# Optimization experiments

Measured on AMD Instinct MI355X. Metric: run time of the kernel, lower is better.

Reference implementation:

```python
import jax, jax.numpy as jnp
import numpy as np

B, S, D_IN = 64, 3072, 128
E, H, OUT = 64, 256, 10
K, STRIDE = 3, 3
T_OUT = (S - K) // STRIDE + 1  # 1024


def setup_inputs() -> dict:
    key = jax.random.key(0)
    ks = jax.random.split(key, 8)
    inputs = jax.random.normal(ks[0], (B, S, D_IN), dtype=jnp.float32)
    r = jnp.zeros((B, E, T_OUT), dtype=jnp.float32)
    s = 0.05
    conv_w = jax.random.normal(ks[1], (E, D_IN, K), dtype=jnp.float32) * s
    conv_b = jax.random.normal(ks[2], (E,), dtype=jnp.float32) * s
    w_ih = jax.random.normal(ks[3], (4 * H, E), dtype=jnp.float32) * s
    w_hh = jax.random.normal(ks[4], (4 * H, H), dtype=jnp.float32) * s
    b_ih = jax.random.normal(ks[5], (4 * H,), dtype=jnp.float32) * s
    b_hh = jax.random.normal(ks[6], (4 * H,), dtype=jnp.float32) * s
    lin_w = jax.random.normal(ks[7], (OUT, H), dtype=jnp.float32) * s
    lin_b = jnp.zeros((OUT,), dtype=jnp.float32)
    return {"inputs": inputs, "r": r, "batch_size": B,
            "conv_w": conv_w, "conv_b": conv_b,
            "w_ih": w_ih, "w_hh": w_hh, "b_ih": b_ih, "b_hh": b_hh,
            "lin_w": lin_w, "lin_b": lin_b}


def _forward(inputs, conv_w, conv_b, w_ih, w_hh, b_ih, b_hh, lin_w, lin_b):
    # F.normalize(inputs, dim=2): L2-normalize feature dim (eps=1e-12)
    norm = jnp.linalg.norm(inputs, axis=2, keepdims=True)
    x = inputs / jnp.maximum(norm, 1e-12)
    # permute(0,2,1): [B, D_IN, S], then Conv1d stride 3
    x = jnp.transpose(x, (0, 2, 1))
    emb = jax.lax.conv_general_dilated(
        x, conv_w, window_strides=(STRIDE,), padding='VALID',
        dimension_numbers=('NCH', 'OIH', 'NCH'))
    emb = emb + conv_b[None, :, None]
    act = jax.nn.relu(emb)                      # [B, E, T_OUT]
    xs = jnp.transpose(act, (2, 0, 1))          # [T, B, E] for scan

    def step(carry, x_t):
        h, c = carry
        gates = x_t @ w_ih.T + b_ih + h @ w_hh.T + b_hh  # [B, 4H]
        i_g, f_g, g_g, o_g = jnp.split(gates, 4, axis=1)
        c_new = jax.nn.sigmoid(f_g) * c + jax.nn.sigmoid(i_g) * jnp.tanh(g_g)
        h_new = jax.nn.sigmoid(o_g) * jnp.tanh(c_new)
        return (h_new, c_new), None

    h0 = jnp.zeros((inputs.shape[0], H), dtype=inputs.dtype)
    c0 = jnp.zeros((inputs.shape[0], H), dtype=inputs.dtype)
    (h_last, _), _ = jax.lax.scan(step, (h0, c0), xs)
    return h_last @ lin_w.T + lin_b             # [B, OUT]


def reference(inputs, r, batch_size, conv_w, conv_b, w_ih, w_hh, b_ih, b_hh, lin_w, lin_b):
    # mode='plain': r and batch_size are unused by the math
    return _forward(inputs, conv_w, conv_b, w_ih, w_hh, b_ih, b_hh, lin_w, lin_b)
```

## Files before the change

### kernel.cpp

```cpp
#include <hip/hip_runtime.h>
#include <math.h>

#define B_   64
#define S_   3072
#define DIN  128
#define E_   64
#define H_   256
#define OUT_ 10
#define T_   1024
#define NG   32
#define GB   2
#define NCH  8
#define NLINES 192
#define SLOT 168

#define ACT_BYTES   (B_*E_*T_*4)
#define HBUF_OFF    ACT_BYTES
#define HBUF_BYTES  (NG*2*NLINES*16)
#define HFINAL_OFF  (HBUF_OFF + HBUF_BYTES)
#define HFINAL_BYTES (NG*GB*H_*4)

typedef float f32x4 __attribute__((ext_vector_type(4)));

__device__ __forceinline__ f32x4 coh_load_f32x4(const float* p) {
  f32x4 r;
  asm volatile("global_load_dwordx4 %0, %1, off sc0 sc1\n\ts_waitcnt vmcnt(0)"
               : "=v"(r) : "v"(p) : "memory");
  return r;
}
__device__ __forceinline__ void coh_store_f32x4(float* p, f32x4 v) {
  asm volatile("global_store_dwordx4 %0, %1, off sc0 sc1" :: "v"(p), "v"(v) : "memory");
}

__device__ __forceinline__ void step_barrier() {
  asm volatile("s_waitcnt lgkmcnt(0)" ::: "memory");
  __builtin_amdgcn_sched_barrier(0);
  __builtin_amdgcn_s_barrier();
}

__device__ __forceinline__ float fast_sigmoid(float x) {
  return __builtin_amdgcn_rcpf(1.0f + __expf(-x));
}
__device__ __forceinline__ float fast_tanh(float x) {
  return 2.0f * __builtin_amdgcn_rcpf(1.0f + __expf(-2.0f * x)) - 1.0f;
}

__global__ __launch_bounds__(512, 1) void conv_kernel(
    const float* __restrict__ in,
    const float* __restrict__ cw,
    const float* __restrict__ cb,
    float* __restrict__ actT)
{
  extern __shared__ float xs[];
  float4* xs4 = (float4*)xs;
  const int bid = blockIdx.x;
  const int b  = bid >> 4;
  const int tb = bid & 15;
  const int tid = threadIdx.x;

  const float4* gin = (const float4*)(in + (size_t)b*S_*DIN + (size_t)tb*192*DIN);
  #pragma unroll
  for (int i = 0; i < 12; ++i) {
    int f4 = tid + i*512;
    int r = f4 >> 5, dq = f4 & 31;
    xs4[r*32 + (dq ^ (r & 7))] = gin[f4];
  }
  __syncthreads();

  const int wv = tid >> 6, ln = tid & 63;
  for (int rr = 0; rr < 24; ++rr) {
    int r = wv*24 + rr;
    int u = r*32 + ((ln >> 1) ^ (r & 7));
    float2* p = (float2*)((char*)xs + (size_t)u*16 + (size_t)(ln & 1)*8);
    float2 v = *p;
    float s = v.x*v.x + v.y*v.y;
    #pragma unroll
    for (int off = 32; off >= 1; off >>= 1) s += __shfl_xor(s, off);
    float inv = 1.0f / fmaxf(sqrtf(s), 1e-12f);
    v.x *= inv; v.y *= inv;
    *p = v;
  }
  __syncthreads();

  const int eo = __builtin_amdgcn_readfirstlane(wv);
  float acc[8];
  #pragma unroll
  for (int j = 0; j < 8; ++j) acc[j] = cb[eo*8 + j];

  const int r0 = 3*ln, r1 = 3*ln + 1, r2 = 3*ln + 2;
  #pragma unroll 4
  for (int dq = 0; dq < 32; ++dq) {
    float4 x0 = xs4[r0*32 + (dq ^ (r0 & 7))];
    float4 x1 = xs4[r1*32 + (dq ^ (r1 & 7))];
    float4 x2 = xs4[r2*32 + (dq ^ (r2 & 7))];
    #pragma unroll
    for (int j = 0; j < 8; ++j) {
      const float* wp = cw + (size_t)(eo*8 + j)*(DIN*3) + dq*12;
      acc[j] += x0.x*wp[0] + x1.x*wp[1] + x2.x*wp[2]
              + x0.y*wp[3] + x1.y*wp[4] + x2.y*wp[5]
              + x0.z*wp[6] + x1.z*wp[7] + x2.z*wp[8]
              + x0.w*wp[9] + x1.w*wp[10] + x2.w*wp[11];
    }
  }

  const int tg = tb*64 + ln;
  #pragma unroll
  for (int j = 0; j < 8; ++j) {
    int e = eo*8 + j;
    actT[(size_t)b*E_*T_ + (size_t)e*T_ + tg] = fmaxf(acc[j], 0.0f);
  }
}

__device__ __forceinline__ void kmap(int hidx, int& kh, int& slot) {
  kh = (hidx < 160) ? 0 : 1;
  slot = (hidx < 160) ? hidx : hidx - 160;
}

__global__ __launch_bounds__(512, 1) void lstm_kernel(
    const float* __restrict__ actT,
    const float* __restrict__ w_ih,
    const float* __restrict__ w_hh,
    const float* __restrict__ b_ih,
    const float* __restrict__ b_hh,
    float* hbuf,
    float* hfinal)
{
  __shared__ float sl[2][2][2][SLOT];

  const int bid = blockIdx.x;
  const int g = bid & 31;
  const int q = bid >> 5;
  const int tid = threadIdx.x;
  const int w = tid >> 6;
  const int l = tid & 63;

  const int khalf = l & 1;
  const int m     = (l >> 1) & 3;
  const int o     = l >> 3;
  const int b     = w & 1;
  const int wh    = w >> 1;
  const int hh    = wh*8 + o;
  const int row   = m*256 + 32*q + hh;

  float4 wv[40];
  if (khalf == 0) {
    const float4* ph = (const float4*)(w_hh + (size_t)row*H_);
    #pragma unroll
    for (int i = 0; i < 40; ++i) wv[i] = ph[i];
  } else {
    const float4* ph = (const float4*)(w_hh + (size_t)row*H_) + 40;
    #pragma unroll
    for (int i = 0; i < 24; ++i) wv[i] = ph[i];
    const float4* px = (const float4*)(w_ih + (size_t)row*E_);
    #pragma unroll
    for (int i = 0; i < 16; ++i) wv[24+i] = px[i];
  }
  const float bias = (khalf == 0) ? (b_ih[row] + b_hh[row]) : 0.0f;

  for (int i = tid; i < 2*2*2*SLOT; i += 512) ((float*)sl)[i] = 0.0f;

  const int ss = l / 24;
  const bool is_store = ((l % 24) == 0);
  const int sline = q*24 + w*3 + ss;
  const int shh0 = wh*8 + 3*ss;
  const int scnt = (ss == 2) ? 2 : 3;

  const bool lane_ok = ((l % 24) != 0);
  const int rank = l - 1 - (l >= 24) - (l >= 48);
  const int pi = w*61 + rank;
  const bool is_poll = (w < 3) && lane_ok && (pi < 168);
  int pline = 0, pb = 0, phh0 = 0, pcnt = 3;
  if (is_poll) {
    int qq = pi / 24;
    int pq = qq + (qq >= q ? 1 : 0);
    int rest = pi % 24;
    int pw = rest / 3, ps = rest % 3;
    pline = pq*24 + pw*3 + ps;
    pb = pw & 1;
    phh0 = 32*pq + (pw >> 1)*8 + 3*ps;
    pcnt = (ps == 2) ? 2 : 3;
  }

  const bool is_x = (tid >= 384);
  const int xi = tid - 384, xb = (xi >> 6) & 1, xe = xi & 63;
  const float* actp = actT + (size_t)((g*GB + xb)*E_ + xe)*T_;

  float* hb = hbuf + (size_t)g*(2*NLINES*4);

  if (is_x) sl[0][xb][1][96 + xe] = actp[0];
  __syncthreads();

  float c = 0.0f;
  for (int t = 0; t < T_; ++t) {
    const int p = t & 1;

    float xval = 0.0f;
    if (is_x) xval = actp[t];

    if (t > 0 && is_poll) {
      const float* lp = hb + (size_t)(p*NLINES + pline)*4;
      f32x4 v = coh_load_f32x4(lp);
      while (__float_as_int(v[3]) != t) v = coh_load_f32x4(lp);
      #pragma unroll
      for (int j = 0; j < 3; ++j) {
        if (j < pcnt) {
          int kh, slot; kmap(phh0 + j, kh, slot);
          sl[p][pb][kh][slot] = v[j];
        }
      }
    }
    if (is_x) sl[p][xb][1][96 + xe] = xval;
    step_barrier();

    float acc = bias;
    {
      const float* hs = &sl[p][b][khalf][0];
      #pragma unroll
      for (int i = 0; i < 40; ++i) {
        float4 h4 = *(const float4*)(hs + i*4);
        acc += wv[i].x*h4.x + wv[i].y*h4.y + wv[i].z*h4.z + wv[i].w*h4.w;
      }
    }

    float ksum = acc + __shfl_xor(acc, 1);
    float x1 = __shfl_xor(ksum, 2);
    float x2 = __shfl_xor(ksum, 4);
    float x3 = __shfl_xor(x1, 4);
    float gi = (m==0)?ksum:(m==1)?x1 :(m==2)?x2 :x3;
    float gf = (m==0)?x1 :(m==1)?ksum:(m==2)?x3 :x2;
    float gg = (m==0)?x2 :(m==1)?x3 :(m==2)?ksum:x1;
    float go = (m==0)?x3 :(m==1)?x2 :(m==2)?x1 :ksum;

    float si = fast_sigmoid(gi);
    float sf = fast_sigmoid(gf);
    float so = fast_sigmoid(go);
    c = sf*c + si*fast_tanh(gg);
    float h = so*fast_tanh(c);

    float v1 = __shfl(h, (l + 8) & 63, 64);
    float v2 = __shfl(h, (l + 16) & 63, 64);
    if (is_store) {
      f32x4 line;
      line[0] = h; line[1] = v1; line[2] = v2;
      line[3] = __int_as_float(t + 1);
      float* dp = hb + (size_t)((((t+1) & 1)*NLINES) + sline)*4;
      coh_store_f32x4(dp, line);
      #pragma unroll
      for (int j = 0; j < 3; ++j) {
        if (j < scnt) {
          int kh, slot; kmap(32*q + shh0 + j, kh, slot);
          sl[p ^ 1][b][kh][slot] = (j == 0) ? h : (j == 1) ? v1 : v2;
        }
      }
      if (t == T_ - 1) {
        #pragma unroll
        for (int j = 0; j < 3; ++j)
          if (j < scnt)
            hfinal[(size_t)g*GB*H_ + (size_t)b*H_ + 32*q + shh0 + j]
                = (j == 0) ? h : (j == 1) ? v1 : v2;
      }
      asm volatile("s_waitcnt vmcnt(0)" ::: "memory");
    }
  }
}

__global__ void head_kernel(const float* __restrict__ hfinal,
                            const float* __restrict__ lw,
                            const float* __restrict__ lb,
                            float* __restrict__ out)
{
  int idx = blockIdx.x*blockDim.x + threadIdx.x;
  if (idx >= B_*OUT_) return;
  int b = idx / OUT_, o = idx % OUT_;
  int g = b >> 1, bl = b & 1;
  const float* h = hfinal + (size_t)g*GB*H_ + (size_t)bl*H_;
  const float* wv = lw + (size_t)o*H_;
  float s = lb[o];
  #pragma unroll 8
  for (int k = 0; k < H_; ++k) s += h[k]*wv[k];
  out[idx] = s;
}

extern "C" void kernel_launch(void* const* d_in, const int* in_sizes, int n_in,
                              void* d_out, int out_size, void* d_ws, size_t ws_size,
                              hipStream_t stream) {
  const float* inputs = (const float*)d_in[0];
  const float* conv_w = (const float*)d_in[3];
  const float* conv_b = (const float*)d_in[4];
  const float* w_ih   = (const float*)d_in[5];
  const float* w_hh   = (const float*)d_in[6];
  const float* b_ih   = (const float*)d_in[7];
  const float* b_hh   = (const float*)d_in[8];
  const float* lin_w  = (const float*)d_in[9];
  const float* lin_b  = (const float*)d_in[10];

  float* actT   = (float*)d_ws;
  float* hbuf   = (float*)((char*)d_ws + HBUF_OFF);
  float* hfinal = (float*)((char*)d_ws + HFINAL_OFF);

  hipMemsetAsync(hbuf, 0, HBUF_BYTES, stream);
  hipLaunchKernelGGL(conv_kernel, dim3(B_*16), dim3(512), 192*128*4, stream,
                     inputs, conv_w, conv_b, actT);
  hipLaunchKernelGGL(lstm_kernel, dim3(NG*NCH), dim3(512), 0, stream,
                     actT, w_ih, w_hh, b_ih, b_hh, hbuf, hfinal);
  hipLaunchKernelGGL(head_kernel, dim3(3), dim3(256), 0, stream,
                     hfinal, lin_w, lin_b, (float*)d_out);
}
```

Measured before the change: 2.201 ms.

## Split x and h LDS buffers, prefetch next x, pipeline coherent polling loads

Separates the input activations into their own double-buffered LDS array and computes the x·W_ih contribution before the cross-block wait, so that work is off the recurrent critical path. The next timestep's x is prefetched into the other buffer. Weights are re-split evenly between k-halves (128 h + 32 x each). Polling now keeps three coherent loads in flight with short sleeps instead of one serialized load-wait loop. The aim is lower per-step latency, at the cost of more complex inline-asm scheduling and extra memory traffic while polling.

```diff
diff --git a/kernel.cpp b/kernel.cpp
--- a/kernel.cpp
+++ b/kernel.cpp
@@ -12,7 +12,6 @@
 #define GB   2
 #define NCH  8
 #define NLINES 192
-#define SLOT 168
 
 #define ACT_BYTES   (B_*E_*T_*4)
 #define HBUF_OFF    ACT_BYTES
@@ -111,11 +110,6 @@
   }
 }
 
-__device__ __forceinline__ void kmap(int hidx, int& kh, int& slot) {
-  kh = (hidx < 160) ? 0 : 1;
-  slot = (hidx < 160) ? hidx : hidx - 160;
-}
-
 __global__ __launch_bounds__(512, 1) void lstm_kernel(
     const float* __restrict__ actT,
     const float* __restrict__ w_ih,
@@ -125,7 +119,8 @@
     float* hbuf,
     float* hfinal)
 {
-  __shared__ float sl[2][2][2][SLOT];
+  __shared__ float hl[2][2][2][132];
+  __shared__ float xl[2][2][64];
 
   const int bid = blockIdx.x;
   const int g = bid & 31;
@@ -143,21 +138,17 @@
   const int row   = m*256 + 32*q + hh;
 
   float4 wv[40];
-  if (khalf == 0) {
-    const float4* ph = (const float4*)(w_hh + (size_t)row*H_);
+  {
+    const float4* ph = (const float4*)(w_hh + (size_t)row*H_) + khalf*32;
     #pragma unroll
-    for (int i = 0; i < 40; ++i) wv[i] = ph[i];
-  } else {
-    const float4* ph = (const float4*)(w_hh + (size_t)row*H_) + 40;
+    for (int i = 0; i < 32; ++i) wv[i] = ph[i];
+    const float4* px = (const float4*)(w_ih + (size_t)row*E_) + khalf*8;
     #pragma unroll
-    for (int i = 0; i < 24; ++i) wv[i] = ph[i];
-    const float4* px = (const float4*)(w_ih + (size_t)row*E_);
-    #pragma unroll
-    for (int i = 0; i < 16; ++i) wv[24+i] = px[i];
+    for (int i = 0; i < 8; ++i) wv[32+i] = px[i];
   }
   const float bias = (khalf == 0) ? (b_ih[row] + b_hh[row]) : 0.0f;
 
-  for (int i = tid; i < 2*2*2*SLOT; i += 512) ((float*)sl)[i] = 0.0f;
+  for (int i = tid; i < 2*2*2*132; i += 512) (&hl[0][0][0][0])[i] = 0.0f;
 
   const int ss = l / 24;
   const bool is_store = ((l % 24) == 0);
@@ -187,37 +178,70 @@
 
   float* hb = hbuf + (size_t)g*(2*NLINES*4);
 
-  if (is_x) sl[0][xb][1][96 + xe] = actp[0];
+  if (is_x) xl[0][xb][xe] = actp[0];
   __syncthreads();
 
   float c = 0.0f;
   for (int t = 0; t < T_; ++t) {
     const int p = t & 1;
 
-    float xval = 0.0f;
-    if (is_x) xval = actp[t];
+    float acc = bias;
+    {
+      const float* xp = &xl[p][b][khalf*32];
+      #pragma unroll
+      for (int i = 0; i < 8; ++i) {
+        float4 x4 = *(const float4*)(xp + 4*i);
+        acc += wv[32+i].x*x4.x + wv[32+i].y*x4.y
+             + wv[32+i].z*x4.z + wv[32+i].w*x4.w;
+      }
+    }
+    if (is_x) {
+      float xv = actp[(t + 1 < T_) ? (t + 1) : t];
+      xl[p ^ 1][xb][xe] = xv;
+    }
 
     if (t > 0 && is_poll) {
       const float* lp = hb + (size_t)(p*NLINES + pline)*4;
-      f32x4 v = coh_load_f32x4(lp);
-      while (__float_as_int(v[3]) != t) v = coh_load_f32x4(lp);
+      f32x4 va, vb, vc, hit = {};
+      asm volatile("global_load_dwordx4 %0, %1, off sc0 sc1" : "=v"(va) : "v"(lp) : "memory");
+      __builtin_amdgcn_s_sleep(4);
+      asm volatile("global_load_dwordx4 %0, %1, off sc0 sc1" : "=v"(vb) : "v"(lp) : "memory");
+      __builtin_amdgcn_s_sleep(4);
+      asm volatile("global_load_dwordx4 %0, %1, off sc0 sc1" : "=v"(vc) : "v"(lp) : "memory");
+      for (;;) {
+        asm volatile("s_waitcnt vmcnt(2)" ::: "memory");
+        __builtin_amdgcn_sched_barrier(0);
+        if (__float_as_int(va[3]) == t) { hit = va; break; }
+        asm volatile("global_load_dwordx4 %0, %1, off sc0 sc1" : "=v"(va) : "v"(lp) : "memory");
+        __builtin_amdgcn_s_sleep(4);
+        asm volatile("s_waitcnt vmcnt(2)" ::: "memory");
+        __builtin_amdgcn_sched_barrier(0);
+        if (__float_as_int(vb[3]) == t) { hit = vb; break; }
+        asm volatile("global_load_dwordx4 %0, %1, off sc0 sc1" : "=v"(vb) : "v"(lp) : "memory");
+        __builtin_amdgcn_s_sleep(4);
+        asm volatile("s_waitcnt vmcnt(2)" ::: "memory");
+        __builtin_amdgcn_sched_barrier(0);
+        if (__float_as_int(vc[3]) == t) { hit = vc; break; }
+        asm volatile("global_load_dwordx4 %0, %1, off sc0 sc1" : "=v"(vc) : "v"(lp) : "memory");
+        __builtin_amdgcn_s_sleep(4);
+      }
+      asm volatile("s_waitcnt vmcnt(0)" ::: "memory");
+      __builtin_amdgcn_sched_barrier(0);
       #pragma unroll
       for (int j = 0; j < 3; ++j) {
         if (j < pcnt) {
-          int kh, slot; kmap(phh0 + j, kh, slot);
-          sl[p][pb][kh][slot] = v[j];
+          int hidx = phh0 + j;
+          hl[p][pb][hidx >> 7][hidx & 127] = hit[j];
         }
       }
     }
-    if (is_x) sl[p][xb][1][96 + xe] = xval;
     step_barrier();
 
-    float acc = bias;
     {
-      const float* hs = &sl[p][b][khalf][0];
+      const float* hs = &hl[p][b][khalf][0];
       #pragma unroll
-      for (int i = 0; i < 40; ++i) {
-        float4 h4 = *(const float4*)(hs + i*4);
+      for (int i = 0; i < 32; ++i) {
+        float4 h4 = *(const float4*)(hs + 4*i);
         acc += wv[i].x*h4.x + wv[i].y*h4.y + wv[i].z*h4.z + wv[i].w*h4.w;
       }
     }
@@ -248,8 +272,8 @@
       #pragma unroll
       for (int j = 0; j < 3; ++j) {
         if (j < scnt) {
-          int kh, slot; kmap(32*q + shh0 + j, kh, slot);
-          sl[p ^ 1][b][kh][slot] = (j == 0) ? h : (j == 1) ? v1 : v2;
+          int hidx = 32*q + shh0 + j;
+          hl[p ^ 1][b][hidx >> 7][hidx & 127] = (j == 0) ? h : (j == 1) ? v1 : v2;
         }
       }
       if (t == T_ - 1) {
```

After: 2.125 ms. 1.04x faster.

## Repartition LSTM to one batch per group across four blocks

Applied to the files above, without the earlier changes.

The recurrent work is split differently across blocks. Before, each group of 8 blocks handled 2 batch rows with 32 hidden units per block. Now each group of 4 blocks handles a single batch row with 64 hidden units per block, keeping the same total block count. This cuts the number of peer blocks each block must poll for hidden-state lines every timestep (3 instead of 7), which shortens the per-step cross-block synchronization. The cost is that each group carries less batch reuse of the weights held in registers, and hbuf/hfinal indexing and the head kernel are adjusted to match.

```diff
diff --git a/kernel.cpp b/kernel.cpp
--- a/kernel.cpp
+++ b/kernel.cpp
@@ -8,17 +8,17 @@
 #define H_   256
 #define OUT_ 10
 #define T_   1024
-#define NG   32
-#define GB   2
-#define NCH  8
-#define NLINES 192
+#define NG   64
+#define NCH  4
+#define NLPW 24
+#define NLINES (NCH*NLPW)
 #define SLOT 168
 
 #define ACT_BYTES   (B_*E_*T_*4)
 #define HBUF_OFF    ACT_BYTES
 #define HBUF_BYTES  (NG*2*NLINES*16)
 #define HFINAL_OFF  (HBUF_OFF + HBUF_BYTES)
-#define HFINAL_BYTES (NG*GB*H_*4)
+#define HFINAL_BYTES (NG*H_*4)
 
 typedef float f32x4 __attribute__((ext_vector_type(4)));
 
@@ -125,11 +125,11 @@
     float* hbuf,
     float* hfinal)
 {
-  __shared__ float sl[2][2][2][SLOT];
+  __shared__ float sl[2][2][SLOT];
 
   const int bid = blockIdx.x;
-  const int g = bid & 31;
-  const int q = bid >> 5;
+  const int g = bid & 63;
+  const int q = bid >> 6;
   const int tid = threadIdx.x;
   const int w = tid >> 6;
   const int l = tid & 63;
@@ -137,10 +137,8 @@
   const int khalf = l & 1;
   const int m     = (l >> 1) & 3;
   const int o     = l >> 3;
-  const int b     = w & 1;
-  const int wh    = w >> 1;
-  const int hh    = wh*8 + o;
-  const int row   = m*256 + 32*q + hh;
+  const int hh    = w*8 + o;
+  const int row   = m*256 + 64*q + hh;
 
   float4 wv[40];
   if (khalf == 0) {
@@ -157,37 +155,35 @@
   }
   const float bias = (khalf == 0) ? (b_ih[row] + b_hh[row]) : 0.0f;
 
-  for (int i = tid; i < 2*2*2*SLOT; i += 512) ((float*)sl)[i] = 0.0f;
+  for (int i = tid; i < 2*2*SLOT; i += 512) ((float*)sl)[i] = 0.0f;
 
   const int ss = l / 24;
   const bool is_store = ((l % 24) == 0);
-  const int sline = q*24 + w*3 + ss;
-  const int shh0 = wh*8 + 3*ss;
+  const int sline = q*NLPW + w*3 + ss;
+  const int shh0 = w*8 + 3*ss;
   const int scnt = (ss == 2) ? 2 : 3;
 
   const bool lane_ok = ((l % 24) != 0);
   const int rank = l - 1 - (l >= 24) - (l >= 48);
   const int pi = w*61 + rank;
-  const bool is_poll = (w < 3) && lane_ok && (pi < 168);
-  int pline = 0, pb = 0, phh0 = 0, pcnt = 3;
+  const bool is_poll = (w < 2) && lane_ok && (pi < 72);
+  int pline = 0, phh0 = 0, pcnt = 3;
   if (is_poll) {
-    int qq = pi / 24;
-    int pq = qq + (qq >= q ? 1 : 0);
-    int rest = pi % 24;
+    int rq = pi / NLPW;
+    int pq = rq + (rq >= q ? 1 : 0);
+    int rest = pi % NLPW;
     int pw = rest / 3, ps = rest % 3;
-    pline = pq*24 + pw*3 + ps;
-    pb = pw & 1;
-    phh0 = 32*pq + (pw >> 1)*8 + 3*ps;
+    pline = pq*NLPW + pw*3 + ps;
+    phh0 = 64*pq + pw*8 + 3*ps;
     pcnt = (ps == 2) ? 2 : 3;
   }
 
-  const bool is_x = (tid >= 384);
-  const int xi = tid - 384, xb = (xi >> 6) & 1, xe = xi & 63;
-  const float* actp = actT + (size_t)((g*GB + xb)*E_ + xe)*T_;
+  const bool is_x = (tid >= 448);
+  const int xe = tid - 448;
+  const float* actp = actT + (size_t)(g*E_ + xe)*T_;
 
   float* hb = hbuf + (size_t)g*(2*NLINES*4);
 
-  if (is_x) sl[0][xb][1][96 + xe] = actp[0];
   __syncthreads();
 
   float c = 0.0f;
@@ -205,19 +201,19 @@
       for (int j = 0; j < 3; ++j) {
         if (j < pcnt) {
           int kh, slot; kmap(phh0 + j, kh, slot);
-          sl[p][pb][kh][slot] = v[j];
+          sl[p][kh][slot] = v[j];
         }
       }
     }
-    if (is_x) sl[p][xb][1][96 + xe] = xval;
+    if (is_x) sl[p][1][96 + xe] = xval;
     step_barrier();
 
     float acc = bias;
     {
-      const float* hs = &sl[p][b][khalf][0];
+      const float* hs = &sl[p][khalf][0];
       #pragma unroll
       for (int i = 0; i < 40; ++i) {
-        float4 h4 = *(const float4*)(hs + i*4);
+        float4 h4 = *(const float4*)(hs + 4*i);
         acc += wv[i].x*h4.x + wv[i].y*h4.y + wv[i].z*h4.z + wv[i].w*h4.w;
       }
     }
@@ -248,15 +244,15 @@
       #pragma unroll
       for (int j = 0; j < 3; ++j) {
         if (j < scnt) {
-          int kh, slot; kmap(32*q + shh0 + j, kh, slot);
-          sl[p ^ 1][b][kh][slot] = (j == 0) ? h : (j == 1) ? v1 : v2;
+          int kh, slot; kmap(64*q + shh0 + j, kh, slot);
+          sl[p ^ 1][kh][slot] = (j == 0) ? h : (j == 1) ? v1 : v2;
         }
       }
       if (t == T_ - 1) {
         #pragma unroll
         for (int j = 0; j < 3; ++j)
           if (j < scnt)
-            hfinal[(size_t)g*GB*H_ + (size_t)b*H_ + 32*q + shh0 + j]
+            hfinal[(size_t)g*H_ + 64*q + shh0 + j]
                 = (j == 0) ? h : (j == 1) ? v1 : v2;
       }
       asm volatile("s_waitcnt vmcnt(0)" ::: "memory");
@@ -272,8 +268,7 @@
   int idx = blockIdx.x*blockDim.x + threadIdx.x;
   if (idx >= B_*OUT_) return;
   int b = idx / OUT_, o = idx % OUT_;
-  int g = b >> 1, bl = b & 1;
-  const float* h = hfinal + (size_t)g*GB*H_ + (size_t)bl*H_;
+  const float* h = hfinal + (size_t)b*H_;
   const float* wv = lw + (size_t)o*H_;
   float s = lb[o];
   #pragma unroll 8
```

Measured after the change: 2.162 ms. No clear change (-1.8%).
